# Performance work log

Hardware: AMD Instinct MI355X
Metric: run time of the kernel (lower is better)

Reference implementation:

```python
import jax, jax.numpy as jnp
import numpy as np
from jax import lax


def conv2d(x, w, b, stride, pad):
    # x: NCHW, w: OIHW (PyTorch Conv2d layout)
    y = lax.conv_general_dilated(x, w, (stride, stride), ((pad, pad), (pad, pad)),
                                 dimension_numbers=('NCHW', 'OIHW', 'NCHW'))
    return y + b[None, :, None, None]


def conv_transpose2d(x, w, b, stride, pad):
    # PyTorch ConvTranspose2d weight layout: (in_ch, out_ch, kH, kW).
    # Equivalent to a conv with lhs dilation, flipped kernel, in/out swapped.
    k = w.shape[2]
    w2 = jnp.transpose(jnp.flip(w, (2, 3)), (1, 0, 2, 3))  # (out, in, k, k)
    p = k - 1 - pad
    y = lax.conv_general_dilated(x, w2, (1, 1), ((p, p), (p, p)),
                                 lhs_dilation=(stride, stride),
                                 dimension_numbers=('NCHW', 'OIHW', 'NCHW'))
    return y + b[None, :, None, None]


def setup_inputs() -> dict:
    key = jax.random.key(0)
    ks = jax.random.split(key, 8)
    K, D = 512, 64  # num_embeddings, embedding_dim
    x = jax.random.uniform(ks[0], (32, 3, 256, 256), jnp.float32)

    def he(k, shape, fan_in):
        return jax.random.normal(k, shape, jnp.float32) * np.float32(np.sqrt(2.0 / fan_in))

    w1 = he(ks[1], (64, 3, 4, 4), 3 * 16);   b1 = jnp.zeros((64,), jnp.float32)
    w2 = he(ks[2], (D, 64, 4, 4), 64 * 16);  b2 = jnp.zeros((D,), jnp.float32)
    # codebook init: uniform(-1/K, 1/K) as in the torch module
    codebook = jax.random.uniform(ks[3], (K, D), jnp.float32, -1.0 / K, 1.0 / K)
    dw1 = he(ks[4], (D, 64, 4, 4), D * 16);  db1 = jnp.zeros((64,), jnp.float32)
    dw2 = he(ks[5], (64, 3, 4, 4), 64 * 16); db2 = jnp.zeros((3,), jnp.float32)
    return dict(x=x, w1=w1, b1=b1, w2=w2, b2=b2, codebook=codebook,
                dw1=dw1, db1=db1, dw2=dw2, db2=db2)


def reference(x, w1, b1, w2, b2, codebook, dw1, db1, dw2, db2):
    # Encoder
    z_e = jax.nn.relu(conv2d(x, w1, b1, 2, 1))
    z_e = jax.nn.relu(conv2d(z_e, w2, b2, 2, 1))  # (N, D, H/4, W/4)
    D = z_e.shape[1]
    # Faithful to torch: .view(-1, C) on contiguous NCHW (NO channel permute)
    zf = z_e.reshape(-1, D)  # (N*Hq*Wq, D) given D == Hq here numerically; rows are contiguous slices
    # ||z - e||^2 = ||z||^2 + ||e||^2 - 2 z.e  -> (M, K) distance matrix
    d = (jnp.sum(zf * zf, axis=1, keepdims=True)
         + jnp.sum(codebook * codebook, axis=1)
         - 2.0 * (zf @ codebook.T))
    idx = jnp.argmin(d, axis=1)           # (M,) int
    z_q = codebook[idx].reshape(z_e.shape)  # gather + reshape back to z_e shape
    # Decoder
    h = jax.nn.relu(conv_transpose2d(z_q, dw1, db1, 2, 1))
    x_recon = jax.nn.sigmoid(conv_transpose2d(h, dw2, db2, 2, 1))
    return x_recon, z_q
```

## Files before the change

kernel.cpp:

```cpp
#include <hip/hip_runtime.h>
#include <math.h>


typedef __attribute__((ext_vector_type(8))) short short8;
typedef __attribute__((ext_vector_type(4))) short short4v;
typedef __attribute__((ext_vector_type(4))) float f32x4;

#define MFMA16(a, b, c) __builtin_amdgcn_mfma_f32_16x16x32_bf16((a), (b), (c), 0, 0, 0)

__device__ __forceinline__ short f2bf(float f) {
  union { float f; unsigned u; } x; x.f = f;
  unsigned r = (x.u + 0x7FFFu + ((x.u >> 16) & 1u)) >> 16;
  return (short)r;
}
__device__ __forceinline__ float bf2f(short s) {
  union { unsigned u; float f; } x;
  x.u = ((unsigned)(unsigned short)s) << 16;
  return x.f;
}

__global__ __launch_bounds__(256) void k_prep(const float* __restrict__ w2,
                                              const float* __restrict__ dw1,
                                              const float* __restrict__ cb,
                                              short* __restrict__ A2,
                                              short* __restrict__ AD1,
                                              short* __restrict__ cbb,
                                              float* __restrict__ cnm) {
  int i = blockIdx.x * 256 + threadIdx.x;
  {
    int t = i >> 12, oc = (i >> 6) & 63, c = i & 63;
    A2[i] = f2bf(w2[(oc * 64 + c) * 16 + t]);
  }
  {
    int p = i >> 14, ab = (i >> 12) & 3, oc = (i >> 6) & 63, c = i & 63;
    int kh = 1 - (p >> 1) + 2 * (ab >> 1);
    int kw = 1 - (p & 1) + 2 * (ab & 1);
    AD1[i] = f2bf(dw1[(c * 64 + oc) * 16 + kh * 4 + kw]);
  }
  if (i < 32768) cbb[i] = f2bf(cb[i]);
  if (i < 512) {
    float s = 0.f;
    for (int d = 0; d < 64; ++d) { float v = cb[i * 64 + d]; s += v * v; }
    cnm[i] = s;
  }
}

__global__ __launch_bounds__(256) void k_conv1(const float* __restrict__ x,
                                               const float* __restrict__ w1,
                                               const float* __restrict__ b1,
                                               short* __restrict__ z1T) {
  __shared__ float sW[3 * 16 * 64];
  __shared__ float sB[64];
  __shared__ float sIn[3 * 34 * 34];
  __shared__ short sOutC[256 * 72];
  const int tid = threadIdx.x;

  for (int i = tid; i < 3072; i += 256) {
    int oc = i & 63, t = (i >> 6) & 15, c = i >> 10;
    sW[i] = w1[(oc * 3 + c) * 16 + t];
  }
  if (tid < 64) sB[tid] = b1[tid];

  const int b = blockIdx.x;
  const int n = b >> 6;
  const int tile = b & 63;
  const int tr = tile >> 3, tc = tile & 7;
  const int oh0 = tr * 16, ow0 = tc * 16;
  const int ih_base = oh0 * 2 - 1, iw_base = ow0 * 2 - 1;

  for (int i = tid; i < 3468; i += 256) {
    int c = i / 1156;
    int rem = i - c * 1156;
    int r = rem / 34;
    int col = rem - r * 34;
    int ih = ih_base + r, iw = iw_base + col;
    float v = 0.f;
    if ((unsigned)ih < 256u && (unsigned)iw < 256u)
      v = x[((n * 3 + c) * 256 + ih) * 256 + iw];
    sIn[i] = v;
  }
  __syncthreads();

  const int ty = tid >> 4, tx = tid & 15;
  float acc[64];
#pragma unroll
  for (int j = 0; j < 64; ++j) acc[j] = sB[j];

  for (int c = 0; c < 3; ++c) {
    for (int t = 0; t < 16; ++t) {
      int kh = t >> 2, kw = t & 3;
      float v = sIn[c * 1156 + (2 * ty + kh) * 34 + (2 * tx + kw)];
      const float4* wp = (const float4*)&sW[(c * 16 + t) * 64];
#pragma unroll
      for (int j = 0; j < 16; ++j) {
        float4 w4 = wp[j];
        acc[4 * j + 0] += v * w4.x;
        acc[4 * j + 1] += v * w4.y;
        acc[4 * j + 2] += v * w4.z;
        acc[4 * j + 3] += v * w4.w;
      }
    }
  }

  const int sp = ty * 16 + tx;
#pragma unroll
  for (int kk = 0; kk < 8; ++kk) {
    short8 v;
#pragma unroll
    for (int t2 = 0; t2 < 8; ++t2) {
      float r = acc[8 * kk + t2];
      v[t2] = f2bf(r > 0.f ? r : 0.f);
    }
    *(short8*)&sOutC[sp * 72 + 8 * kk] = v;
  }
  __syncthreads();
  const int r = tid >> 4, jj = tid & 15;
#pragma unroll
  for (int it = 0; it < 8; ++it) {
    int chunk = jj + 16 * it;
    int owL = chunk >> 3, c8 = chunk & 7;
    short8 v = *(const short8*)&sOutC[(r * 16 + owL) * 72 + 8 * c8];
    *(short8*)(z1T + (((long)(n * 128 + oh0 + r) * 128) + ow0 + owL) * 64 + 8 * c8) = v;
  }
}

__global__ __launch_bounds__(256) void k_conv2(const short* __restrict__ z1T,
                                               const short* __restrict__ A2,
                                               const float* __restrict__ b2,
                                               short* __restrict__ ze) {
  __shared__ char smemC[62400];
  __shared__ float sB2c[64];
  short* slab = (short*)smemC;
  short* sOut = (short*)smemC;

  const int tid = threadIdx.x;
  if (tid < 64) sB2c[tid] = b2[tid];
  const int b = blockIdx.x;
  const int n = b >> 5;
  const int oh0 = (b & 31) * 2;
  const int w = tid >> 6, l = tid & 63;
  const int row = w >> 1, mh = w & 1;
  const int e = l & 15, kg = l >> 4;
  const int ih0 = 2 * oh0 - 1;

  f32x4 acc[2][4];
#pragma unroll
  for (int mi = 0; mi < 2; ++mi)
#pragma unroll
    for (int nt = 0; nt < 4; ++nt) acc[mi][nt] = (f32x4){0.f, 0.f, 0.f, 0.f};

  for (int p = 0; p < 2; ++p) {
    const int c0 = 32 * p;
    __syncthreads();
    for (int i = tid; i < 3120; i += 256) {
      int r = i / 520;
      int rem = i - r * 520;
      int iwL = rem >> 2, li = rem & 3;
      int ih = ih0 + r, iw = iwL - 1;
      short8 v = {0, 0, 0, 0, 0, 0, 0, 0};
      if ((unsigned)ih < 128u && (unsigned)iw < 128u)
        v = *(const short8*)(z1T + (((long)(n * 128 + ih) * 128) + iw) * 64 + c0 + 8 * li);
      *(short8*)&slab[8 * ((r * 130 + iwL) * 5 + li)] = v;
    }
    __syncthreads();

    for (int t = 0; t < 16; ++t) {
      const int kh = t >> 2, kw = t & 3;
      const int rL = 2 * row + kh;
      short8 aF[2], bF[4];
#pragma unroll
      for (int mi = 0; mi < 2; ++mi)
        aF[mi] = *(const short8*)(A2 + ((t * 64 + 32 * mh + 16 * mi + e) * 64) + c0 + 8 * kg);
#pragma unroll
      for (int nt = 0; nt < 4; ++nt) {
        int iwL = 2 * (nt * 16 + e) + kw;
        bF[nt] = *(const short8*)&slab[8 * ((rL * 130 + iwL) * 5 + kg)];
      }
#pragma unroll
      for (int mi = 0; mi < 2; ++mi)
#pragma unroll
        for (int nt = 0; nt < 4; ++nt)
          acc[mi][nt] = MFMA16(aF[mi], bF[nt], acc[mi][nt]);
    }
  }

  __syncthreads();
#pragma unroll
  for (int mi = 0; mi < 2; ++mi)
#pragma unroll
    for (int nt = 0; nt < 4; ++nt)
#pragma unroll
      for (int rr = 0; rr < 4; ++rr) {
        int oc = 32 * mh + 16 * mi + 4 * kg + rr;
        float v = acc[mi][nt][rr] + sB2c[oc];
        sOut[(row * 64 + oc) * 68 + nt * 16 + e] = f2bf(v > 0.f ? v : 0.f);
      }
  __syncthreads();
  {
    int oc = 32 * mh + (l >> 1);
    int half = l & 1;
#pragma unroll
    for (int j = 0; j < 8; ++j) {
      short4v v = *(const short4v*)&sOut[(row * 64 + oc) * 68 + 32 * half + 4 * j];
      *(short4v*)(ze + (((long)(n * 64 + oc) * 64) + oh0 + row) * 64 + 32 * half + 4 * j) = v;
    }
  }
}

__global__ __launch_bounds__(256) void k_vq(const short* __restrict__ zeb,
                                            const short* __restrict__ cbb,
                                            const float* __restrict__ cnm,
                                            const float* __restrict__ cb,
                                            float* __restrict__ zq,
                                            short* __restrict__ zqT) {
  const int tid = threadIdx.x;
  const int wv = tid >> 6, l = tid & 63;
  const int e = l & 15, kg = l >> 4;
  const int b = blockIdx.x;
  const int n = b >> 6, h = b & 63;

  const short* zebase = zeb + (((long)(n * 64 + 16 * wv + e) * 64) + h) * 64;
  short8 aF0 = *(const short8*)(zebase + 8 * kg);
  short8 aF1 = *(const short8*)(zebase + 32 + 8 * kg);

  float bestD[4];
  int bestI[4];
#pragma unroll
  for (int rr = 0; rr < 4; ++rr) { bestD[rr] = 3.4e38f; bestI[rr] = 0; }

  for (int ch = 0; ch < 8; ++ch) {
    f32x4 acc[4];
#pragma unroll
    for (int nt = 0; nt < 4; ++nt) {
      acc[nt] = (f32x4){0.f, 0.f, 0.f, 0.f};
      const short* cbase = cbb + (ch * 64 + nt * 16 + e) * 64;
      short8 b0 = *(const short8*)(cbase + 8 * kg);
      short8 b1 = *(const short8*)(cbase + 32 + 8 * kg);
      acc[nt] = MFMA16(aF0, b0, acc[nt]);
      acc[nt] = MFMA16(aF1, b1, acc[nt]);
    }
#pragma unroll
    for (int nt = 0; nt < 4; ++nt) {
      int code = ch * 64 + nt * 16 + e;
      float cn = cnm[code];
#pragma unroll
      for (int rr = 0; rr < 4; ++rr) {
        float d = cn - 2.f * acc[nt][rr];
        if (d < bestD[rr]) { bestD[rr] = d; bestI[rr] = code; }
      }
    }
  }
#pragma unroll
  for (int m = 1; m <= 8; m <<= 1) {
#pragma unroll
    for (int rr = 0; rr < 4; ++rr) {
      float od = __shfl_xor(bestD[rr], m);
      int oi = __shfl_xor(bestI[rr], m);
      if (od < bestD[rr] || (od == bestD[rr] && oi < bestI[rr])) {
        bestD[rr] = od; bestI[rr] = oi;
      }
    }
  }
#pragma unroll
  for (int rr = 0; rr < 4; ++rr) {
    int c = 16 * wv + 4 * kg + rr;
    int idx = bestI[rr];
    float4 v = *(const float4*)(cb + idx * 64 + 4 * e);
    *(float4*)(zq + (((long)(n * 64 + c) * 64) + h) * 64 + 4 * e) = v;
    short* qt = zqT + (((long)(n * 64 + h) * 64) + 4 * e) * 64 + c;
    qt[0] = f2bf(v.x);
    qt[64] = f2bf(v.y);
    qt[128] = f2bf(v.z);
    qt[192] = f2bf(v.w);
  }
}

__global__ __launch_bounds__(256) void k_deconv1(const short* __restrict__ zqT,
                                                 const short* __restrict__ AD1,
                                                 const float* __restrict__ db1,
                                                 short* __restrict__ hT) {
  __shared__ char smemD[34816];
  __shared__ float sBias[64];
  short* slab = (short*)smemD;
  short* sOut = (short*)smemD;

  const int tid = threadIdx.x;
  if (tid < 64) sBias[tid] = db1[tid];
  const int b = blockIdx.x;
  const int n = b >> 6, i0 = b & 63;
  const int w = tid >> 6, l = tid & 63;
  const int ph = w >> 1, pw = w & 1;
  const int e = l & 15, kg = l >> 4;

  for (int i = tid; i < 1584; i += 256) {
    int r = i / 528;
    int rem = i - r * 528;
    int iwL = rem >> 3, li = rem & 7;
    int ih = i0 - 1 + r, iw = iwL - 1;
    short8 v = {0, 0, 0, 0, 0, 0, 0, 0};
    if ((unsigned)ih < 64u && (unsigned)iw < 64u)
      v = *(const short8*)(zqT + (((long)(n * 64 + ih) * 64) + iw) * 64 + 8 * li);
    *(short8*)&slab[(r * 66 + iwL) * 72 + 8 * li] = v;
  }
  __syncthreads();

  f32x4 acc[4][4];
#pragma unroll
  for (int m = 0; m < 4; ++m)
#pragma unroll
    for (int nt = 0; nt < 4; ++nt) acc[m][nt] = (f32x4){0.f, 0.f, 0.f, 0.f};

  for (int ab = 0; ab < 4; ++ab) {
    const int rL = 1 + ph - (ab >> 1);
    const int coff = pw - (ab & 1) + 1;
#pragma unroll
    for (int ks = 0; ks < 2; ++ks) {
      short8 aF[4], bF[4];
#pragma unroll
      for (int m = 0; m < 4; ++m)
        aF[m] = *(const short8*)(AD1 + (((w * 4 + ab) * 64 + 16 * m + e) * 64) + 32 * ks + 8 * kg);
#pragma unroll
      for (int nt = 0; nt < 4; ++nt) {
        int iwL = nt * 16 + e + coff;
        bF[nt] = *(const short8*)&slab[(rL * 66 + iwL) * 72 + 32 * ks + 8 * kg];
      }
#pragma unroll
      for (int m = 0; m < 4; ++m)
#pragma unroll
        for (int nt = 0; nt < 4; ++nt)
          acc[m][nt] = MFMA16(aF[m], bF[nt], acc[m][nt]);
    }
  }

  __syncthreads();
#pragma unroll
  for (int m = 0; m < 4; ++m)
#pragma unroll
    for (int nt = 0; nt < 4; ++nt) {
      int owIdx = nt * 16 + e;
      int oc0 = 16 * m + 4 * kg;
      short4v o;
#pragma unroll
      for (int rr = 0; rr < 4; ++rr) {
        float v = acc[m][nt][rr] + sBias[oc0 + rr];
        o[rr] = f2bf(v > 0.f ? v : 0.f);
      }
      *(short4v*)&sOut[((w * 64 + owIdx) * 68) + oc0] = o;
    }
  __syncthreads();
  {
    const int oh = 2 * i0 + ph;
    const int ow = 2 * l + pw;
    short* dst = hT + (((long)(n * 128 + oh) * 128) + ow) * 64;
#pragma unroll
    for (int j = 0; j < 16; ++j) {
      short4v v = *(const short4v*)&sOut[((w * 64 + l) * 68) + 4 * j];
      *(short4v*)(dst + 4 * j) = v;
    }
  }
}

__global__ __launch_bounds__(256) void k_deconv2(const short* __restrict__ hT,
                                                 const float* __restrict__ dw2,
                                                 const float* __restrict__ db2,
                                                 float* __restrict__ xr) {
  __shared__ float sW[3072];
  __shared__ float sB2[3];
  __shared__ float sIn[18 * 18 * 9];
  const int tid = threadIdx.x;
  for (int i = tid; i < 3072; i += 256) sW[i] = dw2[i];
  if (tid < 3) sB2[tid] = db2[tid];

  const int b = blockIdx.x;
  const int n = b >> 6, tile = b & 63;
  const int oh0 = (tile >> 3) * 32, ow0 = (tile & 7) * 32;
  const int w = tid >> 6, l = tid & 63;
  const int ph = w >> 1, pw = w & 1;
  const int ihBase = (oh0 >> 1) - 1, iwBase = (ow0 >> 1) - 1;

  int py[4], px[4];
#pragma unroll
  for (int s = 0; s < 4; ++s) {
    int pos = 64 * s + l;
    py[s] = pos >> 4;
    px[s] = pos & 15;
  }
  float acc[4][3];
#pragma unroll
  for (int s = 0; s < 4; ++s) acc[s][0] = acc[s][1] = acc[s][2] = 0.f;

  for (int c0 = 0; c0 < 64; c0 += 8) {
    __syncthreads();
    for (int i = tid; i < 2592; i += 256) {
      int r = i / 144;
      int rem = i - r * 144;
      int col = rem >> 3, cc = rem & 7;
      int ih = ihBase + r, iw = iwBase + col;
      float v = 0.f;
      if ((unsigned)ih < 128u && (unsigned)iw < 128u)
        v = bf2f(hT[(((long)(n * 128 + ih) * 128) + iw) * 64 + c0 + cc]);
      sIn[(r * 18 + col) * 9 + cc] = v;
    }
    __syncthreads();

#pragma unroll
    for (int ab = 0; ab < 4; ++ab) {
      const int a = ab >> 1, bb2 = ab & 1;
      const int t = (1 - ph + 2 * a) * 4 + (1 - pw + 2 * bb2);
      const int dr = ph - a + 1, dc = pw - bb2 + 1;
      for (int cc = 0; cc < 8; ++cc) {
        float w0 = sW[((c0 + cc) * 3 + 0) * 16 + t];
        float w1 = sW[((c0 + cc) * 3 + 1) * 16 + t];
        float w2v = sW[((c0 + cc) * 3 + 2) * 16 + t];
#pragma unroll
        for (int s = 0; s < 4; ++s) {
          float v = sIn[((py[s] + dr) * 18 + px[s] + dc) * 9 + cc];
          acc[s][0] += v * w0;
          acc[s][1] += v * w1;
          acc[s][2] += v * w2v;
        }
      }
    }
  }

#pragma unroll
  for (int s = 0; s < 4; ++s) {
    int oh = oh0 + 2 * py[s] + ph;
    int ow = ow0 + 2 * px[s] + pw;
#pragma unroll
    for (int o = 0; o < 3; ++o) {
      float v = 1.f / (1.f + expf(-(acc[s][o] + sB2[o])));
      xr[(((long)(n * 3 + o) * 256) + oh) * 256 + ow] = v;
    }
  }
}

extern "C" void kernel_launch(void* const* d_in, const int* in_sizes, int n_in,
                              void* d_out, int out_size, void* d_ws, size_t ws_size,
                              hipStream_t stream) {
  (void)in_sizes; (void)n_in; (void)out_size; (void)ws_size;

  const float* x   = (const float*)d_in[0];
  const float* w1  = (const float*)d_in[1];
  const float* b1  = (const float*)d_in[2];
  const float* w2  = (const float*)d_in[3];
  const float* b2  = (const float*)d_in[4];
  const float* cb  = (const float*)d_in[5];
  const float* dw1 = (const float*)d_in[6];
  const float* db1 = (const float*)d_in[7];
  const float* dw2 = (const float*)d_in[8];
  const float* db2 = (const float*)d_in[9];

  char* wsb = (char*)d_ws;
  short* z1T = (short*)wsb;
  short* zeb = (short*)(wsb + 67108864);
  short* zqT = (short*)(wsb + 83886080);
  short* A2  = (short*)(wsb + 100663296);
  short* AD1 = (short*)(wsb + 100794368);
  short* cbb = (short*)(wsb + 100925440);
  float* cnm = (float*)(wsb + 100990976);
  short* hT  = z1T;

  float* xr = (float*)d_out;
  float* zq = (float*)d_out + 6291456;

  k_prep<<<256, 256, 0, stream>>>(w2, dw1, cb, A2, AD1, cbb, cnm);
  k_conv1<<<2048, 256, 0, stream>>>(x, w1, b1, z1T);
  k_conv2<<<1024, 256, 0, stream>>>(z1T, A2, b2, zeb);
  k_vq<<<2048, 256, 0, stream>>>(zeb, cbb, cnm, cb, zq, zqT);
  k_deconv1<<<2048, 256, 0, stream>>>(zqT, AD1, db1, hT);
  k_deconv2<<<2048, 256, 0, stream>>>(hT, dw2, db2, xr);
}
```

Before: 531.3 us.

## Rewrite final transposed conv with bf16 MFMA and padded output channels

Replaces the scalar FP32 FMA loop in the last transposed convolution with bf16 16x16x32 MFMA instructions. The 3 output channels are padded to 16, the input tile is loaded once with vectorized short8 loads instead of an 8-channel-chunked loop, and the sigmoid output is staged in shared memory so stores can be coalesced as float4. Weights are pre-packed into a bf16 AD2 layout in the prep kernel. Most of the MFMA output lanes are wasted on padding, and the larger shared-memory footprint may reduce occupancy.

```diff
diff --git a/kernel.cpp b/kernel.cpp
--- a/kernel.cpp
+++ b/kernel.cpp
@@ -21,9 +21,11 @@
 
 __global__ __launch_bounds__(256) void k_prep(const float* __restrict__ w2,
                                               const float* __restrict__ dw1,
+                                              const float* __restrict__ dw2,
                                               const float* __restrict__ cb,
                                               short* __restrict__ A2,
                                               short* __restrict__ AD1,
+                                              short* __restrict__ AD2,
                                               short* __restrict__ cbb,
                                               float* __restrict__ cnm) {
   int i = blockIdx.x * 256 + threadIdx.x;
@@ -36,6 +38,14 @@
     int kh = 1 - (p >> 1) + 2 * (ab >> 1);
     int kw = 1 - (p & 1) + 2 * (ab & 1);
     AD1[i] = f2bf(dw1[(c * 64 + oc) * 16 + kh * 4 + kw]);
+  }
+  if (i < 16384) {
+    int p = i >> 12, ab = (i >> 10) & 3, oc = (i >> 6) & 15, c = i & 63;
+    int kh = 1 - (p >> 1) + 2 * (ab >> 1);
+    int kw = 1 - (p & 1) + 2 * (ab & 1);
+    short v = 0;
+    if (oc < 3) v = f2bf(dw2[(c * 3 + oc) * 16 + kh * 4 + kw]);
+    AD2[i] = v;
   }
   if (i < 32768) cbb[i] = f2bf(cb[i]);
   if (i < 512) {
@@ -361,77 +371,93 @@
 }
 
 __global__ __launch_bounds__(256) void k_deconv2(const short* __restrict__ hT,
-                                                 const float* __restrict__ dw2,
+                                                 const short* __restrict__ AD2,
                                                  const float* __restrict__ db2,
                                                  float* __restrict__ xr) {
-  __shared__ float sW[3072];
+  __shared__ char smemE[53856];
   __shared__ float sB2[3];
-  __shared__ float sIn[18 * 18 * 9];
+  short* sIn = (short*)smemE;
+  float* sOut = (float*)smemE;
+
   const int tid = threadIdx.x;
-  for (int i = tid; i < 3072; i += 256) sW[i] = dw2[i];
   if (tid < 3) sB2[tid] = db2[tid];
-
   const int b = blockIdx.x;
-  const int n = b >> 6, tile = b & 63;
-  const int oh0 = (tile >> 3) * 32, ow0 = (tile & 7) * 32;
+  const int n = b >> 6;
+  const int rem0 = b & 63;
+  const int q = rem0 >> 1, wh = rem0 & 1;
   const int w = tid >> 6, l = tid & 63;
   const int ph = w >> 1, pw = w & 1;
-  const int ihBase = (oh0 >> 1) - 1, iwBase = (ow0 >> 1) - 1;
-
-  int py[4], px[4];
-#pragma unroll
-  for (int s = 0; s < 4; ++s) {
-    int pos = 64 * s + l;
-    py[s] = pos >> 4;
-    px[s] = pos & 15;
-  }
-  float acc[4][3];
-#pragma unroll
-  for (int s = 0; s < 4; ++s) acc[s][0] = acc[s][1] = acc[s][2] = 0.f;
-
-  for (int c0 = 0; c0 < 64; c0 += 8) {
-    __syncthreads();
-    for (int i = tid; i < 2592; i += 256) {
-      int r = i / 144;
-      int rem = i - r * 144;
-      int col = rem >> 3, cc = rem & 7;
-      int ih = ihBase + r, iw = iwBase + col;
-      float v = 0.f;
-      if ((unsigned)ih < 128u && (unsigned)iw < 128u)
-        v = bf2f(hT[(((long)(n * 128 + ih) * 128) + iw) * 64 + c0 + cc]);
-      sIn[(r * 18 + col) * 9 + cc] = v;
-    }
-    __syncthreads();
-
-#pragma unroll
-    for (int ab = 0; ab < 4; ++ab) {
-      const int a = ab >> 1, bb2 = ab & 1;
-      const int t = (1 - ph + 2 * a) * 4 + (1 - pw + 2 * bb2);
-      const int dr = ph - a + 1, dc = pw - bb2 + 1;
-      for (int cc = 0; cc < 8; ++cc) {
-        float w0 = sW[((c0 + cc) * 3 + 0) * 16 + t];
-        float w1 = sW[((c0 + cc) * 3 + 1) * 16 + t];
-        float w2v = sW[((c0 + cc) * 3 + 2) * 16 + t];
-#pragma unroll
-        for (int s = 0; s < 4; ++s) {
-          float v = sIn[((py[s] + dr) * 18 + px[s] + dc) * 9 + cc];
-          acc[s][0] += v * w0;
-          acc[s][1] += v * w1;
-          acc[s][2] += v * w2v;
+  const int e = l & 15, kg = l >> 4;
+
+  for (int i = tid; i < 3168; i += 256) {
+    int r = i / 528;
+    int rr2 = i - r * 528;
+    int iwL = rr2 >> 3, li = rr2 & 7;
+    int ih = 4 * q - 1 + r, iw = 64 * wh - 1 + iwL;
+    short8 v = {0, 0, 0, 0, 0, 0, 0, 0};
+    if ((unsigned)ih < 128u && (unsigned)iw < 128u)
+      v = *(const short8*)(hT + (((long)(n * 128 + ih) * 128) + iw) * 64 + 8 * li);
+    *(short8*)&sIn[(r * 66 + iwL) * 68 + 8 * li] = v;
+  }
+
+  short8 aF[8];
+#pragma unroll
+  for (int ab = 0; ab < 4; ++ab)
+#pragma unroll
+    for (int chh = 0; chh < 2; ++chh)
+      aF[ab * 2 + chh] = *(const short8*)(AD2 + (((w * 4 + ab) * 16 + e) * 64) + 32 * chh + 8 * kg);
+
+  __syncthreads();
+
+  f32x4 acc[4][4];
+#pragma unroll
+  for (int j = 0; j < 4; ++j)
+#pragma unroll
+    for (int nt = 0; nt < 4; ++nt) acc[j][nt] = (f32x4){0.f, 0.f, 0.f, 0.f};
+
+  const int colBase = e + pw + 1;
+  const int rowBase = 1 + ph;
+
+#pragma unroll
+  for (int ab = 0; ab < 4; ++ab) {
+    const int a = ab >> 1, bb = ab & 1;
+#pragma unroll
+    for (int chh = 0; chh < 2; ++chh) {
+      short8 af = aF[ab * 2 + chh];
+#pragma unroll
+      for (int j = 0; j < 4; ++j) {
+        const int rL = rowBase + j - a;
+#pragma unroll
+        for (int nt = 0; nt < 4; ++nt) {
+          const int iwL = nt * 16 + colBase - bb;
+          short8 bf = *(const short8*)&sIn[(rL * 66 + iwL) * 68 + 32 * chh + 8 * kg];
+          acc[j][nt] = MFMA16(af, bf, acc[j][nt]);
         }
       }
     }
   }
 
-#pragma unroll
-  for (int s = 0; s < 4; ++s) {
-    int oh = oh0 + 2 * py[s] + ph;
-    int ow = ow0 + 2 * px[s] + pw;
-#pragma unroll
-    for (int o = 0; o < 3; ++o) {
-      float v = 1.f / (1.f + expf(-(acc[s][o] + sB2[o])));
-      xr[(((long)(n * 3 + o) * 256) + oh) * 256 + ow] = v;
-    }
+  __syncthreads();
+  if (kg == 0) {
+#pragma unroll
+    for (int j = 0; j < 4; ++j)
+#pragma unroll
+      for (int nt = 0; nt < 4; ++nt) {
+        int ohl = 2 * j + ph;
+        int owl = 2 * (nt * 16 + e) + pw;
+#pragma unroll
+        for (int rr = 0; rr < 3; ++rr) {
+          float v = 1.f / (1.f + expf(-(acc[j][nt][rr] + sB2[rr])));
+          sOut[(rr * 8 + ohl) * 128 + owl] = v;
+        }
+      }
+  }
+  __syncthreads();
+  for (int i = tid; i < 768; i += 256) {
+    int oc = i >> 8, r2 = i & 255;
+    int ohl = r2 >> 5, c4 = r2 & 31;
+    float4 v = ((const float4*)sOut)[i];
+    *(float4*)(xr + (((long)(n * 3 + oc) * 256) + 8 * q + ohl) * 256 + 128 * wh + 4 * c4) = v;
   }
 }
 
@@ -459,15 +485,16 @@
   short* AD1 = (short*)(wsb + 100794368);
   short* cbb = (short*)(wsb + 100925440);
   float* cnm = (float*)(wsb + 100990976);
+  short* AD2 = (short*)(wsb + 100993024);
   short* hT  = z1T;
 
   float* xr = (float*)d_out;
   float* zq = (float*)d_out + 6291456;
 
-  k_prep<<<256, 256, 0, stream>>>(w2, dw1, cb, A2, AD1, cbb, cnm);
+  k_prep<<<256, 256, 0, stream>>>(w2, dw1, dw2, cb, A2, AD1, AD2, cbb, cnm);
   k_conv1<<<2048, 256, 0, stream>>>(x, w1, b1, z1T);
   k_conv2<<<1024, 256, 0, stream>>>(z1T, A2, b2, zeb);
   k_vq<<<2048, 256, 0, stream>>>(zeb, cbb, cnm, cb, zq, zqT);
   k_deconv1<<<2048, 256, 0, stream>>>(zqT, AD1, db1, hT);
-  k_deconv2<<<2048, 256, 0, stream>>>(hT, dw2, db2, xr);
-}
+  k_deconv2<<<2048, 256, 0, stream>>>(hT, AD2, db2, xr);
+}
```

Result: faster. 503.5 us (-5.2%).
